# Optimization experiments

Measured on AMD Instinct MI355X. Metric: run time of the kernel, lower is better.

The kernel has to match this reference:

```python
import jax, jax.numpy as jnp
import numpy as np

B, D, H, E = 1024, 2048, 2048, 16
K = 8            # args.topk
ENERGY_T = 1.0   # args.energy_T
EXP_ID = 0       # args.id (anchor expert)
DROP = 0.2       # hard-coded dropout_coefficient
KEEP = int(K * (1.0 - DROP))  # 6


def setup_inputs() -> dict:
    key = jax.random.key(0)
    ks = jax.random.split(key, 5)
    x = jax.random.normal(ks[0], (B, D), dtype=jnp.float32)
    Wg = jax.random.normal(ks[1], (D, E), dtype=jnp.float32) * 0.02
    bg = jnp.zeros((E,), dtype=jnp.float32)
    We = jax.random.normal(ks[2], (E, D, H), dtype=jnp.float32) * 0.02
    be = jnp.zeros((E, H), dtype=jnp.float32)
    return {"x": x, "Wg": Wg, "bg": bg, "We": We, "be": be}


def reference(x, Wg, bg, We, be):
    # gating: softmax over experts, then top-k (sorted descending, as torch.topk)
    gate = jax.nn.softmax(x @ Wg + bg, axis=-1)          # [B, E]
    vals, idx = jax.lax.top_k(gate, K)                   # [B, K]

    # all expert outputs (E is small; cheaper than gathering [B,K,D,H] weights)
    out_all = jnp.einsum('bd,edh->beh', x, We) + be      # [B, E, H]
    out_k = jnp.take_along_axis(out_all, idx[:, :, None], axis=1)  # [B, K, H]

    # elementwise cosine similarity vs. anchor expert output
    rep = out_all[:, EXP_ID]                             # [B, H]
    cos = (rep[:, None, :] * out_k) / (
        jnp.abs(rep)[:, None, :] * jnp.abs(out_k) + 1e-8)
    cos = jnp.where((idx == EXP_ID)[:, :, None], 1.0, cos)

    # energy/confidence H_k = T * logsumexp(cos / T) over feature dim
    energy = ENERGY_T * jax.nn.logsumexp(cos / ENERGY_T, axis=-1)  # [B, K]

    # keep the KEEP lowest-energy experts (stable sort, as python list.sort)
    keep_pos = jnp.argsort(energy, axis=-1)[:, :KEEP]    # [B, KEEP]
    vals_kept = jnp.take_along_axis(vals, keep_pos, axis=1)           # [B, KEEP]
    out_kept = jnp.take_along_axis(out_k, keep_pos[:, :, None], axis=1)  # [B, KEEP, H]

    return jnp.sum(vals_kept[:, :, None] * out_kept, axis=1)  # [B, H]
```

## Files before the change

### kernel.cpp

```cpp
#include <hip/hip_runtime.h>
#include <math.h>

#define B_ 1024
#define D_ 2048
#define H_ 2048
#define E_ 16
#define K_ 8
#define KEEP_ 6
#define EXP_ID_ 0

typedef double v4d __attribute__((ext_vector_type(4)));

#define WS_OUTALL 0
#define WS_IDX    134217728
#define WS_VALS   (134217728 + 32768)
#define WS_ENERGY (134217728 + 65536)
#define WS_CNT    (134217728 + 98304)
#define WS_ROWS   (134217728 + 98560)
#define WS_ROWTAB (134217728 + 164096)
#define WS_COLTAB (134217728 + 165120)
#define WS_OKFLG  (134217728 + 166144)

__global__ void init_cnt_kernel(int* __restrict__ cnt, int* __restrict__ okflg) {
  if (threadIdx.x < E_) cnt[threadIdx.x] = 0;
  if (threadIdx.x == 0) okflg[0] = 1;
}

__global__ __launch_bounds__(64) void mfma_probe_kernel(
    int* __restrict__ rowtab, int* __restrict__ coltab, int* __restrict__ okflg) {
  const int l = threadIdx.x;
  const v4d z = {0.0, 0.0, 0.0, 0.0};
  double a1 = (double)(l & 15);
  double b1 = ((l >> 4) == 0) ? 1.0 : 0.0;
  v4d d1 = __builtin_amdgcn_mfma_f64_16x16x4f64(a1, b1, z, 0, 0, 0);
  double a2 = ((l >> 4) == 0) ? 1.0 : 0.0;
  double b2 = (double)(l & 15);
  v4d d2 = __builtin_amdgcn_mfma_f64_16x16x4f64(a2, b2, z, 0, 0, 0);
  double a3 = (double)((l & 15) + 1);
  double b3 = (double)((l & 15) + 1);
  v4d d3 = __builtin_amdgcn_mfma_f64_16x16x4f64(a3, b3, z, 0, 0, 0);

  int ok = 1;
#pragma unroll
  for (int g = 0; g < 4; ++g) {
    int r = (int)(d1[g] + 0.5);
    int c = (int)(d2[g] + 0.5);
    if (r < 0 || r > 15 || c < 0 || c > 15) { r = 0; c = 0; ok = 0; }
    rowtab[l * 4 + g] = r;
    coltab[l * 4 + g] = c;
    double expect = 4.0 * (double)(r + 1) * (double)(c + 1);
    if (d3[g] != expect) ok = 0;
  }
  if (!ok) okflg[0] = 0;
}

__global__ __launch_bounds__(64) void gate_kernel(
    const float* __restrict__ x, const float* __restrict__ Wg,
    const float* __restrict__ bg, int* __restrict__ idx, float* __restrict__ vals,
    int* __restrict__ cnt, int* __restrict__ rows) {
  const int b = blockIdx.x;
  const int lane = threadIdx.x;
  double acc[E_];
#pragma unroll
  for (int e = 0; e < E_; ++e) acc[e] = 0.0;
  for (int d = lane; d < D_; d += 64) {
    double xv = (double)x[(size_t)b * D_ + d];
    const float* w = Wg + (size_t)d * E_;
#pragma unroll
    for (int e = 0; e < E_; ++e) acc[e] = fma(xv, (double)w[e], acc[e]);
  }
  for (int off = 32; off > 0; off >>= 1) {
#pragma unroll
    for (int e = 0; e < E_; ++e) acc[e] += __shfl_down(acc[e], off, 64);
  }
  if (lane == 0) {
    double logit[E_];
#pragma unroll
    for (int e = 0; e < E_; ++e) logit[e] = acc[e] + (double)bg[e];
    double m = logit[0];
#pragma unroll
    for (int e = 1; e < E_; ++e) m = fmax(m, logit[e]);
    double p[E_], s = 0.0;
#pragma unroll
    for (int e = 0; e < E_; ++e) { p[e] = exp(logit[e] - m); s += p[e]; }
#pragma unroll
    for (int e = 0; e < E_; ++e) p[e] = p[e] / s;
    unsigned taken = 0;
    for (int j = 0; j < K_; ++j) {
      int best = -1; double bv = -1.0;
#pragma unroll
      for (int e = 0; e < E_; ++e)
        if (!((taken >> e) & 1u) && p[e] > bv) { bv = p[e]; best = e; }
      taken |= (1u << best);
      idx[b * K_ + j] = best;
      vals[b * K_ + j] = (float)bv;
    }
    taken |= 1u;
#pragma unroll
    for (int e = 0; e < E_; ++e) {
      if ((taken >> e) & 1u) {
        int p2 = atomicAdd(&cnt[e], 1);
        rows[e * B_ + p2] = b;
      }
    }
  }
}

#define BM 64
#define BN 64
#define BK 16

__global__ __launch_bounds__(256) void gemm_expert_kernel(
    const float* __restrict__ X, const float* __restrict__ We,
    const float* __restrict__ be, float* __restrict__ out_all,
    const int* __restrict__ cnt, const int* __restrict__ rows,
    const int* __restrict__ rowtab, const int* __restrict__ coltab) {
  const int e  = blockIdx.z;
  const int nrows = cnt[e];
  const int m0 = blockIdx.y * BM;
  if (m0 >= nrows) return;
  const int n0 = blockIdx.x * BN;
  const float* Bmat = We + (size_t)e * D_ * H_;
  const int* rl = rows + e * B_;

  __shared__ double As[BM][BK + 2];
  __shared__ double Bs[BK][BN + 2];

  const int tid = threadIdx.x;
  const int arow  = tid >> 2;
  const int acol4 = (tid & 3) * 4;
  const int brow  = tid >> 4;
  const int bcol4 = (tid & 15) * 4;

  const int gidx = m0 + arow;
  const int grow = rl[(gidx < nrows) ? gidx : (nrows - 1)];
  const float* aptr = X + (size_t)grow * D_;
  const float* bptr = Bmat + (size_t)brow * H_ + n0 + bcol4;

  const int lane = tid & 63;
  const int wave = tid >> 6;
  const int lr = lane & 15;
  const int lq = lane >> 4;

  v4d acc[4];
#pragma unroll
  for (int c = 0; c < 4; ++c) acc[c] = (v4d){0.0, 0.0, 0.0, 0.0};

  float4 av = *(const float4*)(aptr + acol4);
  float4 bv = *(const float4*)(bptr);

  for (int k0 = 0; k0 < D_; k0 += BK) {
    __syncthreads();
    *(double2*)&As[arow][acol4 + 0] = make_double2((double)av.x, (double)av.y);
    *(double2*)&As[arow][acol4 + 2] = make_double2((double)av.z, (double)av.w);
    *(double2*)&Bs[brow][bcol4 + 0] = make_double2((double)bv.x, (double)bv.y);
    *(double2*)&Bs[brow][bcol4 + 2] = make_double2((double)bv.z, (double)bv.w);
    __syncthreads();
    if (k0 + BK < D_) {
      av = *(const float4*)(aptr + (k0 + BK) + acol4);
      bv = *(const float4*)(bptr + (size_t)(k0 + BK) * H_);
    }
#pragma unroll
    for (int k4 = 0; k4 < BK; k4 += 4) {
      double a = As[wave * 16 + lr][k4 + lq];
#pragma unroll
      for (int c = 0; c < 4; ++c) {
        double bb = Bs[k4 + lq][c * 16 + lr];
        acc[c] = __builtin_amdgcn_mfma_f64_16x16x4f64(a, bb, acc[c], 0, 0, 0);
      }
    }
  }
  int drow[4], dcol[4];
#pragma unroll
  for (int g = 0; g < 4; ++g) {
    drow[g] = rowtab[lane * 4 + g];
    dcol[g] = coltab[lane * 4 + g];
  }
#pragma unroll
  for (int c = 0; c < 4; ++c) {
#pragma unroll
    for (int g = 0; g < 4; ++g) {
      const int ridx = m0 + wave * 16 + drow[g];
      if (ridx < nrows) {
        const int mrow = rl[ridx];
        const int col = n0 + c * 16 + dcol[g];
        out_all[((size_t)mrow * E_ + e) * H_ + col] =
            (float)(acc[c][g] + (double)be[(size_t)e * H_ + col]);
      }
    }
  }
}

__global__ __launch_bounds__(256) void energy_kernel(
    const float* __restrict__ out_all, const int* __restrict__ idx,
    float* __restrict__ energy) {
  const int b = blockIdx.x, j = blockIdx.y, t = threadIdx.x;
  const int e = idx[b * K_ + j];
  if (e == EXP_ID_) {
    if (t == 0) energy[b * K_ + j] = 1.0f + (float)log(2048.0);
    return;
  }
  const float* rep = out_all + ((size_t)b * E_ + EXP_ID_) * H_;
  const float* ok  = out_all + ((size_t)b * E_ + e) * H_;

  __shared__ float cs[H_];
  __shared__ float red[256];
  __shared__ float chain[128];

  float mx = -2.0f;
  for (int h = t; h < H_; h += 256) {
    float r = rep[h], o = ok[h];
    float num = r * o;
    float den = fabsf(r) * fabsf(o) + 1e-8f;
    float c = num / den;
    cs[h] = c;
    mx = fmaxf(mx, c);
  }
  red[t] = mx;
  __syncthreads();
  for (int off = 128; off > 0; off >>= 1) {
    if (t < off) red[t] = fmaxf(red[t], red[t + off]);
    __syncthreads();
  }
  const float m = red[0];
  __syncthreads();

  if (t < 128) {
    const int blk = t >> 3, jj = t & 7;
    const float* base = cs + blk * 128;
    float d0 = base[jj] - m;
    float r = (float)exp((double)d0);
#pragma unroll
    for (int q = 1; q < 16; ++q) {
      float dq = base[q * 8 + jj] - m;
      float term = (float)exp((double)dq);
      r = r + term;
    }
    chain[t] = r;
  }
  __syncthreads();

  if (t == 0) {
    float Bsum[16];
#pragma unroll
    for (int blk = 0; blk < 16; ++blk) {
      const float* c8 = chain + blk * 8;
      float s01 = c8[0] + c8[1];
      float s23 = c8[2] + c8[3];
      float s45 = c8[4] + c8[5];
      float s67 = c8[6] + c8[7];
      Bsum[blk] = (s01 + s23) + (s45 + s67);
    }
    float C[8], D[4], Ee[2];
#pragma unroll
    for (int i = 0; i < 8; ++i) C[i] = Bsum[2 * i] + Bsum[2 * i + 1];
#pragma unroll
    for (int i = 0; i < 4; ++i) D[i] = C[2 * i] + C[2 * i + 1];
#pragma unroll
    for (int i = 0; i < 2; ++i) Ee[i] = D[2 * i] + D[2 * i + 1];
    float S = Ee[0] + Ee[1];
    energy[b * K_ + j] = m + (float)log((double)S);
  }
}

__global__ __launch_bounds__(256) void final_kernel(
    const float* __restrict__ out_all, const int* __restrict__ idx,
    const float* __restrict__ vals, const float* __restrict__ energy,
    float* __restrict__ out) {
  const int b = blockIdx.x;
  const int h = blockIdx.y * 256 + threadIdx.x;
  float En[K_];
#pragma unroll
  for (int j = 0; j < K_; ++j) En[j] = energy[b * K_ + j];
  double s = 0.0;
#pragma unroll
  for (int j = 0; j < K_; ++j) {
    int pos = 0;
#pragma unroll
    for (int j2 = 0; j2 < K_; ++j2)
      pos += (En[j2] < En[j]) || (En[j2] == En[j] && j2 < j);
    if (pos < KEEP_) {
      int e = idx[b * K_ + j];
      s += (double)vals[b * K_ + j] *
           (double)out_all[((size_t)b * E_ + e) * H_ + h];
    }
  }
  out[(size_t)b * H_ + h] = (float)s;
}

extern "C" void kernel_launch(void* const* d_in, const int* in_sizes, int n_in,
                              void* d_out, int out_size, void* d_ws, size_t ws_size,
                              hipStream_t stream) {
  const float* x  = (const float*)d_in[0];
  const float* Wg = (const float*)d_in[1];
  const float* bg = (const float*)d_in[2];
  const float* We = (const float*)d_in[3];
  const float* be = (const float*)d_in[4];
  float* out = (float*)d_out;

  char* ws = (char*)d_ws;
  float* out_all = (float*)(ws + WS_OUTALL);
  int*   idx     = (int*)(ws + WS_IDX);
  float* vals    = (float*)(ws + WS_VALS);
  float* energy  = (float*)(ws + WS_ENERGY);
  int*   cnt     = (int*)(ws + WS_CNT);
  int*   rows    = (int*)(ws + WS_ROWS);
  int*   rowtab  = (int*)(ws + WS_ROWTAB);
  int*   coltab  = (int*)(ws + WS_COLTAB);
  int*   okflg   = (int*)(ws + WS_OKFLG);

  init_cnt_kernel<<<dim3(1), dim3(64), 0, stream>>>(cnt, okflg);

  mfma_probe_kernel<<<dim3(1), dim3(64), 0, stream>>>(rowtab, coltab, okflg);

  gate_kernel<<<dim3(B_), dim3(64), 0, stream>>>(x, Wg, bg, idx, vals, cnt, rows);

  gemm_expert_kernel<<<dim3(H_ / BN, B_ / BM, E_), dim3(256), 0, stream>>>(
      x, We, be, out_all, cnt, rows, rowtab, coltab);

  energy_kernel<<<dim3(B_, K_), dim3(256), 0, stream>>>(out_all, idx, energy);

  final_kernel<<<dim3(B_, H_ / 256), dim3(256), 0, stream>>>(
      out_all, idx, vals, energy, out);
}
```

Measured before the change: 1.483 ms.

## Load MFMA operands directly from global memory, dropping LDS staging in expert GEMM

The expert GEMM no longer stages A and B tiles through shared memory with double-buffered prefetch and barriers. Each lane now reads its scalar A and B fragments straight from global memory every k-step and feeds them to the f64 MFMA. This removes the LDS writes, LDS reads and __syncthreads, but each of the four waves now reloads the same B tile on its own, and the loads are scalar and strided by H, so reuse now depends on the caches and load latency is exposed.

```diff
diff --git a/kernel.cpp b/kernel.cpp
--- a/kernel.cpp
+++ b/kernel.cpp
@@ -108,7 +108,6 @@
 
 #define BM 64
 #define BN 64
-#define BK 16
 
 __global__ __launch_bounds__(256) void gemm_expert_kernel(
     const float* __restrict__ X, const float* __restrict__ We,
@@ -123,53 +122,36 @@
   const float* Bmat = We + (size_t)e * D_ * H_;
   const int* rl = rows + e * B_;
 
-  __shared__ double As[BM][BK + 2];
-  __shared__ double Bs[BK][BN + 2];
-
-  const int tid = threadIdx.x;
-  const int arow  = tid >> 2;
-  const int acol4 = (tid & 3) * 4;
-  const int brow  = tid >> 4;
-  const int bcol4 = (tid & 15) * 4;
-
-  const int gidx = m0 + arow;
-  const int grow = rl[(gidx < nrows) ? gidx : (nrows - 1)];
-  const float* aptr = X + (size_t)grow * D_;
-  const float* bptr = Bmat + (size_t)brow * H_ + n0 + bcol4;
-
+  const int tid  = threadIdx.x;
   const int lane = tid & 63;
   const int wave = tid >> 6;
   const int lr = lane & 15;
   const int lq = lane >> 4;
 
+  const int ridx = m0 + wave * 16 + lr;
+  const int grow = rl[(ridx < nrows) ? ridx : (nrows - 1)];
+  const float* arow = X + (size_t)grow * D_;
+  const float* bbase = Bmat + (size_t)lq * H_ + n0 + lr;
+
   v4d acc[4];
 #pragma unroll
   for (int c = 0; c < 4; ++c) acc[c] = (v4d){0.0, 0.0, 0.0, 0.0};
 
-  float4 av = *(const float4*)(aptr + acol4);
-  float4 bv = *(const float4*)(bptr);
-
-  for (int k0 = 0; k0 < D_; k0 += BK) {
-    __syncthreads();
-    *(double2*)&As[arow][acol4 + 0] = make_double2((double)av.x, (double)av.y);
-    *(double2*)&As[arow][acol4 + 2] = make_double2((double)av.z, (double)av.w);
-    *(double2*)&Bs[brow][bcol4 + 0] = make_double2((double)bv.x, (double)bv.y);
-    *(double2*)&Bs[brow][bcol4 + 2] = make_double2((double)bv.z, (double)bv.w);
-    __syncthreads();
-    if (k0 + BK < D_) {
-      av = *(const float4*)(aptr + (k0 + BK) + acol4);
-      bv = *(const float4*)(bptr + (size_t)(k0 + BK) * H_);
-    }
-#pragma unroll
-    for (int k4 = 0; k4 < BK; k4 += 4) {
-      double a = As[wave * 16 + lr][k4 + lq];
-#pragma unroll
-      for (int c = 0; c < 4; ++c) {
-        double bb = Bs[k4 + lq][c * 16 + lr];
-        acc[c] = __builtin_amdgcn_mfma_f64_16x16x4f64(a, bb, acc[c], 0, 0, 0);
-      }
-    }
-  }
+#pragma unroll 4
+  for (int k4 = 0; k4 < D_; k4 += 4) {
+    const float* bp = bbase + (size_t)k4 * H_;
+    float af  = arow[k4 + lq];
+    float bf0 = bp[0];
+    float bf1 = bp[16];
+    float bf2 = bp[32];
+    float bf3 = bp[48];
+    double a = (double)af;
+    acc[0] = __builtin_amdgcn_mfma_f64_16x16x4f64(a, (double)bf0, acc[0], 0, 0, 0);
+    acc[1] = __builtin_amdgcn_mfma_f64_16x16x4f64(a, (double)bf1, acc[1], 0, 0, 0);
+    acc[2] = __builtin_amdgcn_mfma_f64_16x16x4f64(a, (double)bf2, acc[2], 0, 0, 0);
+    acc[3] = __builtin_amdgcn_mfma_f64_16x16x4f64(a, (double)bf3, acc[3], 0, 0, 0);
+  }
+
   int drow[4], dcol[4];
 #pragma unroll
   for (int g = 0; g < 4; ++g) {
@@ -180,9 +162,9 @@
   for (int c = 0; c < 4; ++c) {
 #pragma unroll
     for (int g = 0; g < 4; ++g) {
-      const int ridx = m0 + wave * 16 + drow[g];
-      if (ridx < nrows) {
-        const int mrow = rl[ridx];
+      const int rix = m0 + wave * 16 + drow[g];
+      if (rix < nrows) {
+        const int mrow = rl[rix];
         const int col = n0 + c * 16 + dcol[g];
         out_all[((size_t)mrow * E_ + e) * H_ + col] =
             (float)(acc[c][g] + (double)be[(size_t)e * H_ + col]);
```

Result: slower. 1.616 ms (+8.9%).

## Double-buffer expert GEMM shared tiles and store them as float

Applied to the files above, without the earlier changes.

The expert GEMM now keeps two shared-memory tile buffers and alternates between them. This removes one of the two barriers per K-tile and lets global loads for the next tile overlap MFMA work on the current one. Tiles are stored in LDS as fp32 and widened to fp64 when read, which halves LDS footprint and store traffic. The cost is a conversion on every operand read and more complex loop control.

```diff
diff --git a/kernel.cpp b/kernel.cpp
--- a/kernel.cpp
+++ b/kernel.cpp
@@ -123,8 +123,8 @@
   const float* Bmat = We + (size_t)e * D_ * H_;
   const int* rl = rows + e * B_;
 
-  __shared__ double As[BM][BK + 2];
-  __shared__ double Bs[BK][BN + 2];
+  __shared__ float As[2][BM][BK + 4];
+  __shared__ float Bs[2][BK][BN + 4];
 
   const int tid = threadIdx.x;
   const int arow  = tid >> 2;
@@ -148,28 +148,41 @@
 
   float4 av = *(const float4*)(aptr + acol4);
   float4 bv = *(const float4*)(bptr);
-
-  for (int k0 = 0; k0 < D_; k0 += BK) {
+  *(float4*)&As[0][arow][acol4] = av;
+  *(float4*)&Bs[0][brow][bcol4] = bv;
+
+#define COMPUTE_TILE(BUF)                                                    \
+  _Pragma("unroll")                                                          \
+  for (int k4 = 0; k4 < BK; k4 += 4) {                                       \
+    double a = (double)As[BUF][wave * 16 + lr][k4 + lq];                     \
+    _Pragma("unroll")                                                        \
+    for (int c = 0; c < 4; ++c) {                                            \
+      double bb = (double)Bs[BUF][k4 + lq][c * 16 + lr];                     \
+      acc[c] = __builtin_amdgcn_mfma_f64_16x16x4f64(a, bb, acc[c], 0, 0, 0); \
+    }                                                                        \
+  }
+
+  for (int k0 = 0; k0 < D_; k0 += 2 * BK) {
     __syncthreads();
-    *(double2*)&As[arow][acol4 + 0] = make_double2((double)av.x, (double)av.y);
-    *(double2*)&As[arow][acol4 + 2] = make_double2((double)av.z, (double)av.w);
-    *(double2*)&Bs[brow][bcol4 + 0] = make_double2((double)bv.x, (double)bv.y);
-    *(double2*)&Bs[brow][bcol4 + 2] = make_double2((double)bv.z, (double)bv.w);
+    av = *(const float4*)(aptr + (k0 + BK) + acol4);
+    bv = *(const float4*)(bptr + (size_t)(k0 + BK) * H_);
+    COMPUTE_TILE(0)
+    *(float4*)&As[1][arow][acol4] = av;
+    *(float4*)&Bs[1][brow][bcol4] = bv;
     __syncthreads();
-    if (k0 + BK < D_) {
-      av = *(const float4*)(aptr + (k0 + BK) + acol4);
-      bv = *(const float4*)(bptr + (size_t)(k0 + BK) * H_);
-    }
-#pragma unroll
-    for (int k4 = 0; k4 < BK; k4 += 4) {
-      double a = As[wave * 16 + lr][k4 + lq];
-#pragma unroll
-      for (int c = 0; c < 4; ++c) {
-        double bb = Bs[k4 + lq][c * 16 + lr];
-        acc[c] = __builtin_amdgcn_mfma_f64_16x16x4f64(a, bb, acc[c], 0, 0, 0);
-      }
-    }
-  }
+    const bool more = (k0 + 2 * BK) < D_;
+    if (more) {
+      av = *(const float4*)(aptr + (k0 + 2 * BK) + acol4);
+      bv = *(const float4*)(bptr + (size_t)(k0 + 2 * BK) * H_);
+    }
+    COMPUTE_TILE(1)
+    if (more) {
+      *(float4*)&As[0][arow][acol4] = av;
+      *(float4*)&Bs[0][brow][bcol4] = bv;
+    }
+  }
+#undef COMPUTE_TILE
+
   int drow[4], dcol[4];
 #pragma unroll
   for (int g = 0; g < 4; ++g) {
@@ -180,9 +193,9 @@
   for (int c = 0; c < 4; ++c) {
 #pragma unroll
     for (int g = 0; g < 4; ++g) {
-      const int ridx = m0 + wave * 16 + drow[g];
-      if (ridx < nrows) {
-        const int mrow = rl[ridx];
+      const int rix = m0 + wave * 16 + drow[g];
+      if (rix < nrows) {
+        const int mrow = rl[rix];
         const int col = n0 + c * 16 + dcol[g];
         out_all[((size_t)mrow * E_ + e) * H_ + col] =
             (float)(acc[c][g] + (double)be[(size_t)e * H_ + col]);
```

Measured after the change: 1.469 ms. No clear change (-1.0%).
